# Optimization experiments

Hardware: AMD Instinct MI355X
Metric: run time of the kernel (lower is better)

The kernel has to match this reference:

```python
import jax, jax.numpy as jnp
import numpy as np

K_SIZE = 5
PAD = 2  # (dilation*(k-1)+1-stride+1)//2 with dilation=stride=1
DEPTH_MAX = 10.0
SAMPLE_NUM = 40
AREA_TYPE = 1
AREA_THRED = 0.0  # k_size**2 * 0.5 * 0.0


def _select_index(k_size=K_SIZE, sample_num=SAMPLE_NUM, area_thred=AREA_THRED,
                  area_type=AREA_TYPE, seed=0):
    """Faithful port of AdaptiveDepth2normal.select_index (host-side, deterministic seed)."""
    rng = np.random.RandomState(seed)
    num = k_size ** 2
    p1 = rng.choice(num, sample_num, replace=True); rng.shuffle(p1)
    p2 = rng.choice(num, sample_num, replace=True); rng.shuffle(p2)
    p3 = rng.choice(num, sample_num, replace=True); rng.shuffle(p3)
    index_list = np.stack([p1, p2, p3], axis=1)
    valid_list, seen, areas = [], set(), []
    for row in index_list:
        a, b, c = np.sort(row)
        if (a, b, c) in seen:
            continue
        ax, ay = a % k_size, a // k_size
        bx, by = b % k_size, b // k_size
        cx, cy = c % k_size, c // k_size
        # NOTE: /2 applies only to second term, exactly as in the original code
        area = (bx - ax) * (cy - ay) - (by - ay) * (cx - ax) / 2
        if area > area_thred:
            valid_list.append([a, b, c]); seen.add((a, b, c)); areas.append(area)
        elif area < -area_thred:
            valid_list.append([a, c, b]); seen.add((a, c, b)); areas.append(-area)
    tri = np.asarray(valid_list, dtype=np.int32)              # [nn, 3]
    w = np.asarray(areas, dtype=np.float64) ** area_type
    return tri, (w / w.sum()).astype(np.float32)


def _unfold(x, k=K_SIZE, pad=PAD):
    """torch.nn.Unfold(k, padding=pad, stride=1): x [B,C,H,W] -> [B,C,k*k,H,W], kh-major order."""
    B, C, H, W = x.shape
    xp = jnp.pad(x, ((0, 0), (0, 0), (pad, pad), (pad, pad)))
    return jnp.stack([xp[:, :, dy:dy + H, dx:dx + W]
                      for dy in range(k) for dx in range(k)], axis=2)


def setup_inputs() -> dict:
    key = jax.random.key(0)
    k1, k2 = jax.random.split(key)
    B, H, W = 2, 384, 512
    depth = jax.random.uniform(k1, (B, 1, H, W), dtype=jnp.float32) * 8.0 + 0.5  # in (0, depth_max)
    Kmat = jnp.array([[500.0, 0.0, W / 2.0],
                      [0.0, 500.0, H / 2.0],
                      [0.0, 0.0, 1.0]], dtype=jnp.float32)
    intrinsic = jnp.tile(Kmat[None], (B, 1, 1))
    guide_weight = jax.random.uniform(k2, (B, H, W, K_SIZE * K_SIZE), dtype=jnp.float32)
    tri, aw = _select_index()
    return {"depth": depth, "intrinsic": intrinsic, "guide_weight": guide_weight,
            "triangle_index": jnp.asarray(tri), "triangle_area_weights": jnp.asarray(aw)}


def reference(depth, intrinsic, guide_weight, triangle_index, triangle_area_weights):
    d = depth[:, 0]                                  # [B,H,W]
    B, H, W = d.shape
    Kinv = jnp.linalg.inv(intrinsic)                 # [B,3,3]
    jj = jnp.arange(W, dtype=d.dtype)
    ii = jnp.arange(H, dtype=d.dtype)
    coords = jnp.stack([jnp.broadcast_to(jj[None, :], (H, W)),
                        jnp.broadcast_to(ii[:, None], (H, W)),
                        jnp.ones((H, W), d.dtype)], axis=0)  # [3,H,W] (u,v,1)
    points = jnp.einsum('bij,jhw->bihw', Kinv, coords) * d[:, None]  # [B,3,H,W]

    pp = _unfold(points).transpose(0, 3, 4, 2, 1)    # [B,H,W,25,3]
    p1 = jnp.take(pp, triangle_index[:, 0], axis=3)  # [B,H,W,nn,3]
    p2 = jnp.take(pp, triangle_index[:, 1], axis=3)
    p3 = jnp.take(pp, triangle_index[:, 2], axis=3)
    n = jnp.cross(p2 - p1, p3 - p1)                  # [B,H,W,nn,3]
    n = n / (jnp.linalg.norm(n, axis=-1, keepdims=True) + 1e-5)

    valid = ((d > 0) & (d < DEPTH_MAX)).astype(d.dtype)          # [B,H,W]
    vp = _unfold(valid[:, None])[:, 0].transpose(0, 2, 3, 1)     # [B,H,W,25]
    v_tri = (jnp.take(vp, triangle_index[:, 0], axis=3)
             * jnp.take(vp, triangle_index[:, 1], axis=3)
             * jnp.take(vp, triangle_index[:, 2], axis=3))       # [B,H,W,nn]
    g_tri = (jnp.take(guide_weight, triangle_index[:, 0], axis=3)
             * jnp.take(guide_weight, triangle_index[:, 1], axis=3)
             * jnp.take(guide_weight, triangle_index[:, 2], axis=3))
    fw = v_tri * triangle_area_weights[None, None, None, :] * g_tri  # if_area=True, if_pa=True
    fw = jax.nn.softmax(fw, axis=-1)
    nw = jnp.sum(n * fw[..., None], axis=3)                      # [B,H,W,3]
    nw = nw / (jnp.linalg.norm(nw, axis=-1, keepdims=True) + 1e-5)
    out = jnp.where(valid[..., None] > 0, nw, jnp.zeros((), d.dtype))
    return out.transpose(0, 3, 1, 2), points
```

## Files before the change

kernel.cpp:

```cpp
#include <hip/hip_runtime.h>
#include <math.h>

#define KSZ 5
#define PADR 2
#define TILE_W 32
#define TILE_H 8
#define HALO_W (TILE_W + 2*PADR)
#define HALO_H (TILE_H + 2*PADR)
#define HALO_N (HALO_H * HALO_W)
#define MAX_TRI 128
#define NTHREADS 256

__device__ __forceinline__ float eigen_pexp(float x) {
    float m = floorf(__fmaf_rn(x, 1.44269504088896341f, 0.5f));
    float r = __fmaf_rn(-m, 0.693359375f, x);
    r = __fmaf_rn(-m, -2.12194440e-4f, r);
    float r2 = __fmul_rn(r, r);
    float p = 1.9875691500E-4f;
    p = __fmaf_rn(p, r, 1.3981999507E-3f);
    p = __fmaf_rn(p, r, 8.3334519073E-3f);
    p = __fmaf_rn(p, r, 4.1665795894E-2f);
    p = __fmaf_rn(p, r, 1.6666665459E-1f);
    p = __fmaf_rn(p, r, 5.0000001201E-1f);
    p = __fmaf_rn(p, r2, r);
    p = __fadd_rn(p, 1.0f);
    return ldexpf(p, (int)m);
}

__global__ __launch_bounds__(NTHREADS)
void d2n_kernel(const float* __restrict__ depth,
                const float* __restrict__ intrinsic,
                const float* __restrict__ guide,
                const int* __restrict__ tri,
                const float* __restrict__ aw,
                float* __restrict__ out_n,
                float* __restrict__ out_p,
                int B, int H, int W, int T)
{
    __shared__ float4 s_pts[HALO_N];
    __shared__ float  s_gw[TILE_H * TILE_W * (KSZ*KSZ)];

    const int tid = threadIdx.x;
    const int tx  = tid & (TILE_W - 1);
    const int ty  = tid >> 5;
    const int b   = blockIdx.z;
    const int w0  = blockIdx.x * TILE_W;
    const int h0  = blockIdx.y * TILE_H;

    const float* Km = intrinsic + b * 9;
    const double a00=Km[0], a01=Km[1], a02=Km[2];
    const double a10=Km[3], a11=Km[4], a12=Km[5];
    const double a20=Km[6], a21=Km[7], a22=Km[8];
    const double det = a00*(a11*a22-a12*a21) - a01*(a10*a22-a12*a20) + a02*(a10*a21-a11*a20);
    const double id  = 1.0 / det;
    const float i00 = (float)((a11*a22-a12*a21)*id), i01 = (float)((a02*a21-a01*a22)*id), i02 = (float)((a01*a12-a02*a11)*id);
    const float i10 = (float)((a12*a20-a10*a22)*id), i11 = (float)((a00*a22-a02*a20)*id), i12 = (float)((a02*a10-a00*a12)*id);
    const float i20 = (float)((a10*a21-a11*a20)*id), i21 = (float)((a01*a20-a00*a21)*id), i22 = (float)((a00*a11-a01*a10)*id);

    for (int i = tid; i < HALO_N; i += NTHREADS) {
        int r  = i / HALO_W;
        int c  = i - r * HALO_W;
        int hh = h0 + r - PADR;
        int ww = w0 + c - PADR;
        float4 v = make_float4(0.f, 0.f, 0.f, 0.f);
        if (hh >= 0 && hh < H && ww >= 0 && ww < W) {
            float d  = depth[(size_t)(b * H + hh) * W + ww];
            float fj = (float)ww, fi = (float)hh;
            float sx = __fadd_rn(__fadd_rn(__fmul_rn(i00, fj), __fmul_rn(i01, fi)), i02);
            float sy = __fadd_rn(__fadd_rn(__fmul_rn(i10, fj), __fmul_rn(i11, fi)), i12);
            float sz = __fadd_rn(__fadd_rn(__fmul_rn(i20, fj), __fmul_rn(i21, fi)), i22);
            v.x = __fmul_rn(sx, d);
            v.y = __fmul_rn(sy, d);
            v.z = __fmul_rn(sz, d);
            v.w = (d > 0.f && d < 10.f) ? 1.f : 0.f;
        }
        s_pts[i] = v;
    }

    const int GW_TOT = TILE_H * TILE_W * (KSZ*KSZ);
    for (int i = tid; i < GW_TOT; i += NTHREADS) {
        int r   = i / (TILE_W * KSZ*KSZ);
        int rem = i - r * (TILE_W * KSZ*KSZ);
        int hh  = h0 + r;
        float val = 0.f;
        if (hh < H)
            val = guide[((size_t)(b * H + hh) * W + w0) * (KSZ*KSZ) + rem];
        s_gw[i] = val;
    }

    __syncthreads();

    const int base = ty * HALO_W + tx;
    const int ctr  = base + PADR * HALO_W + PADR;
    float* gw_pix = &s_gw[(ty * TILE_W + tx) * (KSZ*KSZ)];
    const float4 pcv = s_pts[ctr];
    const float  cv  = pcv.w;

    #pragma unroll
    for (int k = 0; k < KSZ*KSZ; ++k) {
        const int o = base + (k / KSZ) * HALO_W + (k % KSZ);
        gw_pix[k] = __fmul_rn(gw_pix[k], s_pts[o].w);
    }

    const int Tl = T < MAX_TRI ? T : MAX_TRI;

    float r0=0.f, r1=0.f, r2=0.f, r3=0.f, r4=0.f, r5=0.f, r6=0.f, r7=0.f;
    float axv = 0.f, ayv = 0.f, azv = 0.f;

    auto body = [&](int t, float& racc) {
        int j1 = tri[3*t], j2 = tri[3*t+1], j3 = tri[3*t+2];
        float awt = aw[t];
        int o1 = base + (j1 / KSZ) * HALO_W + (j1 - (j1 / KSZ) * KSZ);
        int o2 = base + (j2 / KSZ) * HALO_W + (j2 - (j2 / KSZ) * KSZ);
        int o3 = base + (j3 / KSZ) * HALO_W + (j3 - (j3 / KSZ) * KSZ);
        float g = __fmul_rn(__fmul_rn(gw_pix[j1], gw_pix[j2]), gw_pix[j3]);
        float f = __fmul_rn(g, awt);
        float e = eigen_pexp(f);
        racc = __fadd_rn(racc, e);
        float4 p1 = s_pts[o1], p2 = s_pts[o2], p3 = s_pts[o3];
        float e1x = __fsub_rn(p2.x, p1.x), e1y = __fsub_rn(p2.y, p1.y), e1z = __fsub_rn(p2.z, p1.z);
        float e2x = __fsub_rn(p3.x, p1.x), e2y = __fsub_rn(p3.y, p1.y), e2z = __fsub_rn(p3.z, p1.z);
        float t1 = __fmul_rn(e1z, e2y);
        float nx = __fmaf_rn(e1y, e2z, -t1);
        float t2 = __fmul_rn(e1x, e2z);
        float ny = __fmaf_rn(e1z, e2x, -t2);
        float t3 = __fmul_rn(e1y, e2x);
        float nz = __fmaf_rn(e1x, e2y, -t3);
        float q   = __fmaf_rn(nx, nx, __fmaf_rn(ny, ny, __fmul_rn(nz, nz)));
        float den = __fadd_rn(__builtin_amdgcn_sqrtf(q), 1e-5f);
        float inv = __builtin_amdgcn_rcpf(den);
        float ew  = __fmul_rn(e, inv);
        axv = __fmaf_rn(nx, ew, axv);
        ayv = __fmaf_rn(ny, ew, ayv);
        azv = __fmaf_rn(nz, ew, azv);
    };

    const int nmain = (Tl >= 8) ? (Tl & ~7) : 0;
    for (int tb = 0; tb < nmain; tb += 8) {
        body(tb+0, r0); body(tb+1, r1); body(tb+2, r2); body(tb+3, r3);
        body(tb+4, r4); body(tb+5, r5); body(tb+6, r6); body(tb+7, r7);
    }
    float s = 0.f;
    if (Tl >= 8)
        s = __fadd_rn(__fadd_rn(__fadd_rn(r0, r1), __fadd_rn(r2, r3)),
                      __fadd_rn(__fadd_rn(r4, r5), __fadd_rn(r6, r7)));
    for (int t = nmain; t < Tl; ++t) body(t, s);

    float nwx = __fdiv_rn(axv, s);
    float nwy = __fdiv_rn(ayv, s);
    float nwz = __fdiv_rn(azv, s);
    float q2   = __fmaf_rn(nwx, nwx, __fmaf_rn(nwy, nwy, __fmul_rn(nwz, nwz)));
    float den2 = __fadd_rn(__fsqrt_rn(q2), 1e-5f);
    float ox = __fdiv_rn(nwx, den2);
    float oy = __fdiv_rn(nwy, den2);
    float oz = __fdiv_rn(nwz, den2);
    if (cv <= 0.f) { ox = 0.f; oy = 0.f; oz = 0.f; }

    const int hh = h0 + ty, ww = w0 + tx;
    if (hh < H && ww < W) {
        const size_t hw = (size_t)H * W;
        const size_t p0 = (size_t)b * 3 * hw + (size_t)hh * W + ww;
        out_n[p0]        = ox;
        out_n[p0 + hw]   = oy;
        out_n[p0 + 2*hw] = oz;
        out_p[p0]        = pcv.x;
        out_p[p0 + hw]   = pcv.y;
        out_p[p0 + 2*hw] = pcv.z;
    }
}

extern "C" void kernel_launch(void* const* d_in, const int* in_sizes, int n_in,
                              void* d_out, int out_size, void* d_ws, size_t ws_size,
                              hipStream_t stream) {
    const float* depth = (const float*)d_in[0];
    const float* intr  = (const float*)d_in[1];
    const float* guide = (const float*)d_in[2];
    const int*   tri   = (const int*)d_in[3];
    const float* aw    = (const float*)d_in[4];

    const int B = in_sizes[1] / 9;
    const int T = in_sizes[4];
    const int H = 384, W = 512;

    float* out_n = (float*)d_out;
    float* out_p = out_n + (size_t)B * 3 * H * W;

    dim3 grid((W + TILE_W - 1) / TILE_W, (H + TILE_H - 1) / TILE_H, B);
    d2n_kernel<<<grid, NTHREADS, 0, stream>>>(depth, intr, guide, tri, aw,
                                              out_n, out_p, B, H, W, T);
}
```

Measured before the change: 48.53 us.

## Compute two pixels per thread with split SoA LDS layout and taller tiles

New measurement: 60.26 us. 24.2% more time.

```diff
diff --git a/kernel.cpp b/kernel.cpp
--- a/kernel.cpp
+++ b/kernel.cpp
@@ -4,10 +4,12 @@
 #define KSZ 5
 #define PADR 2
 #define TILE_W 32
-#define TILE_H 8
+#define TILE_H 16
 #define HALO_W (TILE_W + 2*PADR)
 #define HALO_H (TILE_H + 2*PADR)
 #define HALO_N (HALO_H * HALO_W)
+#define X2ST 37
+#define GVST 260
 #define MAX_TRI 128
 #define NTHREADS 256
 
@@ -27,7 +29,7 @@
     return ldexpf(p, (int)m);
 }
 
-__global__ __launch_bounds__(NTHREADS)
+__global__ __launch_bounds__(NTHREADS, 2)
 void d2n_kernel(const float* __restrict__ depth,
                 const float* __restrict__ intrinsic,
                 const float* __restrict__ guide,
@@ -37,12 +39,13 @@
                 float* __restrict__ out_p,
                 int B, int H, int W, int T)
 {
-    __shared__ float4 s_pts[HALO_N];
-    __shared__ float  s_gw[TILE_H * TILE_W * (KSZ*KSZ)];
+    __shared__ float2 sX[HALO_H * X2ST];
+    __shared__ float2 sY[HALO_H * X2ST];
+    __shared__ float2 sZ[HALO_H * X2ST];
+    __shared__ float  sV[HALO_N];
+    __shared__ float2 sG[25 * GVST];
 
     const int tid = threadIdx.x;
-    const int tx  = tid & (TILE_W - 1);
-    const int ty  = tid >> 5;
     const int b   = blockIdx.z;
     const int w0  = blockIdx.x * TILE_W;
     const int h0  = blockIdx.y * TILE_H;
@@ -57,115 +60,160 @@
     const float i10 = (float)((a12*a20-a10*a22)*id), i11 = (float)((a00*a22-a02*a20)*id), i12 = (float)((a02*a10-a00*a12)*id);
     const float i20 = (float)((a10*a21-a11*a20)*id), i21 = (float)((a01*a20-a00*a21)*id), i22 = (float)((a00*a11-a01*a10)*id);
 
+    float* Xd = (float*)sX; float* Yd = (float*)sY; float* Zd = (float*)sZ;
     for (int i = tid; i < HALO_N; i += NTHREADS) {
-        int r  = i / HALO_W;
-        int c  = i - r * HALO_W;
-        int hh = h0 + r - PADR;
-        int ww = w0 + c - PADR;
-        float4 v = make_float4(0.f, 0.f, 0.f, 0.f);
+        int hr = i / HALO_W;
+        int hc = i - hr * HALO_W;
+        int hh = h0 + hr - PADR;
+        int ww = w0 + hc - PADR;
+        float x = 0.f, y = 0.f, z = 0.f, v = 0.f;
         if (hh >= 0 && hh < H && ww >= 0 && ww < W) {
             float d  = depth[(size_t)(b * H + hh) * W + ww];
             float fj = (float)ww, fi = (float)hh;
             float sx = __fadd_rn(__fadd_rn(__fmul_rn(i00, fj), __fmul_rn(i01, fi)), i02);
             float sy = __fadd_rn(__fadd_rn(__fmul_rn(i10, fj), __fmul_rn(i11, fi)), i12);
             float sz = __fadd_rn(__fadd_rn(__fmul_rn(i20, fj), __fmul_rn(i21, fi)), i22);
-            v.x = __fmul_rn(sx, d);
-            v.y = __fmul_rn(sy, d);
-            v.z = __fmul_rn(sz, d);
-            v.w = (d > 0.f && d < 10.f) ? 1.f : 0.f;
+            x = __fmul_rn(sx, d);
+            y = __fmul_rn(sy, d);
+            z = __fmul_rn(sz, d);
+            v = (d > 0.f && d < 10.f) ? 1.f : 0.f;
         }
-        s_pts[i] = v;
-    }
-
-    const int GW_TOT = TILE_H * TILE_W * (KSZ*KSZ);
-    for (int i = tid; i < GW_TOT; i += NTHREADS) {
-        int r   = i / (TILE_W * KSZ*KSZ);
-        int rem = i - r * (TILE_W * KSZ*KSZ);
-        int hh  = h0 + r;
-        float val = 0.f;
-        if (hh < H)
-            val = guide[((size_t)(b * H + hh) * W + w0) * (KSZ*KSZ) + rem];
-        s_gw[i] = val;
-    }
-
+        int da = hr * (2 * X2ST) + 2 * hc;
+        Xd[da] = x; Yd[da] = y; Zd[da] = z;
+        if (hc > 0) { Xd[da-1] = x; Yd[da-1] = y; Zd[da-1] = z; }
+        sV[i] = v;
+    }
     __syncthreads();
 
-    const int base = ty * HALO_W + tx;
-    const int ctr  = base + PADR * HALO_W + PADR;
-    float* gw_pix = &s_gw[(ty * TILE_W + tx) * (KSZ*KSZ)];
-    const float4 pcv = s_pts[ctr];
-    const float  cv  = pcv.w;
-
-    #pragma unroll
-    for (int k = 0; k < KSZ*KSZ; ++k) {
-        const int o = base + (k / KSZ) * HALO_W + (k % KSZ);
-        gw_pix[k] = __fmul_rn(gw_pix[k], s_pts[o].w);
-    }
+    float* Gd = (float*)sG;
+    for (int i = tid; i < TILE_H * TILE_W * 25; i += NTHREADS) {
+        int row = i / (TILE_W * 25);
+        int rem = i - row * (TILE_W * 25);
+        int col = rem / 25;
+        int k   = rem - col * 25;
+        int hh  = h0 + row;
+        float val = (hh < H)
+            ? guide[((size_t)(b * H + hh) * W + w0) * 25 + rem] : 0.f;
+        int kd = k / 5, km = k - 5 * kd;
+        float pv = sV[(row + kd) * HALO_W + (col + km)];
+        Gd[k * (2 * GVST) + row * TILE_W + col] = __fmul_rn(val, pv);
+    }
+    __syncthreads();
+
+    const int l   = tid & 63;
+    const int wv  = tid >> 6;
+    const int row = wv * 4 + (l >> 4);
+    const int lx  = l & 15;
+    const int col = 2 * lx;
+    const int pb  = row * X2ST + col;
+    const int gb  = (row << 4) + lx;
 
     const int Tl = T < MAX_TRI ? T : MAX_TRI;
 
-    float r0=0.f, r1=0.f, r2=0.f, r3=0.f, r4=0.f, r5=0.f, r6=0.f, r7=0.f;
-    float axv = 0.f, ayv = 0.f, azv = 0.f;
-
-    auto body = [&](int t, float& racc) {
+    float r0a=0.f,r1a=0.f,r2a=0.f,r3a=0.f,r4a=0.f,r5a=0.f,r6a=0.f,r7a=0.f;
+    float r0b=0.f,r1b=0.f,r2b=0.f,r3b=0.f,r4b=0.f,r5b=0.f,r6b=0.f,r7b=0.f;
+    float axa=0.f, aya=0.f, aza=0.f, axb=0.f, ayb=0.f, azb=0.f;
+
+    auto body = [&](int t, float& ra, float& rb) {
         int j1 = tri[3*t], j2 = tri[3*t+1], j3 = tri[3*t+2];
         float awt = aw[t];
-        int o1 = base + (j1 / KSZ) * HALO_W + (j1 - (j1 / KSZ) * KSZ);
-        int o2 = base + (j2 / KSZ) * HALO_W + (j2 - (j2 / KSZ) * KSZ);
-        int o3 = base + (j3 / KSZ) * HALO_W + (j3 - (j3 / KSZ) * KSZ);
-        float g = __fmul_rn(__fmul_rn(gw_pix[j1], gw_pix[j2]), gw_pix[j3]);
-        float f = __fmul_rn(g, awt);
-        float e = eigen_pexp(f);
-        racc = __fadd_rn(racc, e);
-        float4 p1 = s_pts[o1], p2 = s_pts[o2], p3 = s_pts[o3];
-        float e1x = __fsub_rn(p2.x, p1.x), e1y = __fsub_rn(p2.y, p1.y), e1z = __fsub_rn(p2.z, p1.z);
-        float e2x = __fsub_rn(p3.x, p1.x), e2y = __fsub_rn(p3.y, p1.y), e2z = __fsub_rn(p3.z, p1.z);
-        float t1 = __fmul_rn(e1z, e2y);
-        float nx = __fmaf_rn(e1y, e2z, -t1);
-        float t2 = __fmul_rn(e1x, e2z);
-        float ny = __fmaf_rn(e1z, e2x, -t2);
-        float t3 = __fmul_rn(e1y, e2x);
-        float nz = __fmaf_rn(e1x, e2y, -t3);
-        float q   = __fmaf_rn(nx, nx, __fmaf_rn(ny, ny, __fmul_rn(nz, nz)));
-        float den = __fadd_rn(__builtin_amdgcn_sqrtf(q), 1e-5f);
-        float inv = __builtin_amdgcn_rcpf(den);
-        float ew  = __fmul_rn(e, inv);
-        axv = __fmaf_rn(nx, ew, axv);
-        ayv = __fmaf_rn(ny, ew, ayv);
-        azv = __fmaf_rn(nz, ew, azv);
+        int d1 = (j1 / KSZ) * X2ST + (j1 - (j1 / KSZ) * KSZ);
+        int d2 = (j2 / KSZ) * X2ST + (j2 - (j2 / KSZ) * KSZ);
+        int d3 = (j3 / KSZ) * X2ST + (j3 - (j3 / KSZ) * KSZ);
+        float2 G1 = sG[j1 * GVST + gb];
+        float2 G2 = sG[j2 * GVST + gb];
+        float2 G3 = sG[j3 * GVST + gb];
+        float2 x1 = sX[pb + d1], y1 = sY[pb + d1], z1 = sZ[pb + d1];
+        float2 x2 = sX[pb + d2], y2 = sY[pb + d2], z2 = sZ[pb + d2];
+        float2 x3 = sX[pb + d3], y3 = sY[pb + d3], z3 = sZ[pb + d3];
+        {
+            float g = __fmul_rn(__fmul_rn(G1.x, G2.x), G3.x);
+            float f = __fmul_rn(g, awt);
+            float e = eigen_pexp(f);
+            ra = __fadd_rn(ra, e);
+            float e1x = __fsub_rn(x2.x, x1.x), e1y = __fsub_rn(y2.x, y1.x), e1z = __fsub_rn(z2.x, z1.x);
+            float e2x = __fsub_rn(x3.x, x1.x), e2y = __fsub_rn(y3.x, y1.x), e2z = __fsub_rn(z3.x, z1.x);
+            float t1 = __fmul_rn(e1z, e2y);
+            float nx = __fmaf_rn(e1y, e2z, -t1);
+            float t2 = __fmul_rn(e1x, e2z);
+            float ny = __fmaf_rn(e1z, e2x, -t2);
+            float t3 = __fmul_rn(e1y, e2x);
+            float nz = __fmaf_rn(e1x, e2y, -t3);
+            float q   = __fmaf_rn(nx, nx, __fmaf_rn(ny, ny, __fmul_rn(nz, nz)));
+            float den = __fadd_rn(__builtin_amdgcn_sqrtf(q), 1e-5f);
+            float inv = __builtin_amdgcn_rcpf(den);
+            float ew  = __fmul_rn(e, inv);
+            axa = __fmaf_rn(nx, ew, axa);
+            aya = __fmaf_rn(ny, ew, aya);
+            aza = __fmaf_rn(nz, ew, aza);
+        }
+        {
+            float g = __fmul_rn(__fmul_rn(G1.y, G2.y), G3.y);
+            float f = __fmul_rn(g, awt);
+            float e = eigen_pexp(f);
+            rb = __fadd_rn(rb, e);
+            float e1x = __fsub_rn(x2.y, x1.y), e1y = __fsub_rn(y2.y, y1.y), e1z = __fsub_rn(z2.y, z1.y);
+            float e2x = __fsub_rn(x3.y, x1.y), e2y = __fsub_rn(y3.y, y1.y), e2z = __fsub_rn(z3.y, z1.y);
+            float t1 = __fmul_rn(e1z, e2y);
+            float nx = __fmaf_rn(e1y, e2z, -t1);
+            float t2 = __fmul_rn(e1x, e2z);
+            float ny = __fmaf_rn(e1z, e2x, -t2);
+            float t3 = __fmul_rn(e1y, e2x);
+            float nz = __fmaf_rn(e1x, e2y, -t3);
+            float q   = __fmaf_rn(nx, nx, __fmaf_rn(ny, ny, __fmul_rn(nz, nz)));
+            float den = __fadd_rn(__builtin_amdgcn_sqrtf(q), 1e-5f);
+            float inv = __builtin_amdgcn_rcpf(den);
+            float ew  = __fmul_rn(e, inv);
+            axb = __fmaf_rn(nx, ew, axb);
+            ayb = __fmaf_rn(ny, ew, ayb);
+            azb = __fmaf_rn(nz, ew, azb);
+        }
     };
 
     const int nmain = (Tl >= 8) ? (Tl & ~7) : 0;
     for (int tb = 0; tb < nmain; tb += 8) {
-        body(tb+0, r0); body(tb+1, r1); body(tb+2, r2); body(tb+3, r3);
-        body(tb+4, r4); body(tb+5, r5); body(tb+6, r6); body(tb+7, r7);
-    }
-    float s = 0.f;
-    if (Tl >= 8)
-        s = __fadd_rn(__fadd_rn(__fadd_rn(r0, r1), __fadd_rn(r2, r3)),
-                      __fadd_rn(__fadd_rn(r4, r5), __fadd_rn(r6, r7)));
-    for (int t = nmain; t < Tl; ++t) body(t, s);
-
-    float nwx = __fdiv_rn(axv, s);
-    float nwy = __fdiv_rn(ayv, s);
-    float nwz = __fdiv_rn(azv, s);
+        body(tb+0, r0a, r0b); body(tb+1, r1a, r1b);
+        body(tb+2, r2a, r2b); body(tb+3, r3a, r3b);
+        body(tb+4, r4a, r4b); body(tb+5, r5a, r5b);
+        body(tb+6, r6a, r6b); body(tb+7, r7a, r7b);
+    }
+    float sa = 0.f, sb = 0.f;
+    if (Tl >= 8) {
+        sa = __fadd_rn(__fadd_rn(__fadd_rn(r0a, r1a), __fadd_rn(r2a, r3a)),
+                       __fadd_rn(__fadd_rn(r4a, r5a), __fadd_rn(r6a, r7a)));
+        sb = __fadd_rn(__fadd_rn(__fadd_rn(r0b, r1b), __fadd_rn(r2b, r3b)),
+                       __fadd_rn(__fadd_rn(r4b, r5b), __fadd_rn(r6b, r7b)));
+    }
+    for (int t = nmain; t < Tl; ++t) body(t, sa, sb);
+
+    const float2 cx2 = sX[(row + PADR) * X2ST + col + PADR];
+    const float2 cy2 = sY[(row + PADR) * X2ST + col + PADR];
+    const float2 cz2 = sZ[(row + PADR) * X2ST + col + PADR];
+    const float  cva = sV[(row + PADR) * HALO_W + col + PADR];
+    const float  cvb = sV[(row + PADR) * HALO_W + col + PADR + 1];
+
+    float nwx = __fdiv_rn(axa, sa), nwy = __fdiv_rn(aya, sa), nwz = __fdiv_rn(aza, sa);
     float q2   = __fmaf_rn(nwx, nwx, __fmaf_rn(nwy, nwy, __fmul_rn(nwz, nwz)));
     float den2 = __fadd_rn(__fsqrt_rn(q2), 1e-5f);
-    float ox = __fdiv_rn(nwx, den2);
-    float oy = __fdiv_rn(nwy, den2);
-    float oz = __fdiv_rn(nwz, den2);
-    if (cv <= 0.f) { ox = 0.f; oy = 0.f; oz = 0.f; }
-
-    const int hh = h0 + ty, ww = w0 + tx;
-    if (hh < H && ww < W) {
+    float oxa = __fdiv_rn(nwx, den2), oya = __fdiv_rn(nwy, den2), oza = __fdiv_rn(nwz, den2);
+    if (cva <= 0.f) { oxa = 0.f; oya = 0.f; oza = 0.f; }
+
+    nwx = __fdiv_rn(axb, sb); nwy = __fdiv_rn(ayb, sb); nwz = __fdiv_rn(azb, sb);
+    q2   = __fmaf_rn(nwx, nwx, __fmaf_rn(nwy, nwy, __fmul_rn(nwz, nwz)));
+    den2 = __fadd_rn(__fsqrt_rn(q2), 1e-5f);
+    float oxb = __fdiv_rn(nwx, den2), oyb = __fdiv_rn(nwy, den2), ozb = __fdiv_rn(nwz, den2);
+    if (cvb <= 0.f) { oxb = 0.f; oyb = 0.f; ozb = 0.f; }
+
+    const int hh = h0 + row, ww = w0 + col;
+    if (hh < H && ww + 1 < W) {
         const size_t hw = (size_t)H * W;
         const size_t p0 = (size_t)b * 3 * hw + (size_t)hh * W + ww;
-        out_n[p0]        = ox;
-        out_n[p0 + hw]   = oy;
-        out_n[p0 + 2*hw] = oz;
-        out_p[p0]        = pcv.x;
-        out_p[p0 + hw]   = pcv.y;
-        out_p[p0 + 2*hw] = pcv.z;
+        *(float2*)&out_n[p0]          = make_float2(oxa, oxb);
+        *(float2*)&out_n[p0 + hw]     = make_float2(oya, oyb);
+        *(float2*)&out_n[p0 + 2*hw]   = make_float2(oza, ozb);
+        *(float2*)&out_p[p0]          = make_float2(cx2.x, cx2.y);
+        *(float2*)&out_p[p0 + hw]     = make_float2(cy2.x, cy2.y);
+        *(float2*)&out_p[p0 + 2*hw]   = make_float2(cz2.x, cz2.y);
     }
 }
 
```

## Split point unprojection into a separate pass with padded global buffer

Applied to the files above, without the earlier changes.

Measured after the change: 47.29 us. 1.03x faster.

```diff
diff --git a/kernel.cpp b/kernel.cpp
--- a/kernel.cpp
+++ b/kernel.cpp
@@ -28,14 +28,163 @@
 }
 
 __global__ __launch_bounds__(NTHREADS)
-void d2n_kernel(const float* __restrict__ depth,
+void pts_kernel(const float* __restrict__ depth,
                 const float* __restrict__ intrinsic,
-                const float* __restrict__ guide,
-                const int* __restrict__ tri,
-                const float* __restrict__ aw,
-                float* __restrict__ out_n,
+                float4* __restrict__ pts,
                 float* __restrict__ out_p,
-                int B, int H, int W, int T)
+                int B, int H, int W)
+{
+    const int HP = H + 2*PADR, WP = W + 2*PADR;
+    const int total = B * HP * WP;
+    int idx = blockIdx.x * NTHREADS + threadIdx.x;
+    if (idx >= total) return;
+    int b   = idx / (HP * WP);
+    int rem = idx - b * (HP * WP);
+    int pr  = rem / WP;
+    int pc  = rem - pr * WP;
+    int hh  = pr - PADR;
+    int ww  = pc - PADR;
+
+    const float* Km = intrinsic + b * 9;
+    const double a00=Km[0], a01=Km[1], a02=Km[2];
+    const double a10=Km[3], a11=Km[4], a12=Km[5];
+    const double a20=Km[6], a21=Km[7], a22=Km[8];
+    const double det = a00*(a11*a22-a12*a21) - a01*(a10*a22-a12*a20) + a02*(a10*a21-a11*a20);
+    const double id  = 1.0 / det;
+    const float i00 = (float)((a11*a22-a12*a21)*id), i01 = (float)((a02*a21-a01*a22)*id), i02 = (float)((a01*a12-a02*a11)*id);
+    const float i10 = (float)((a12*a20-a10*a22)*id), i11 = (float)((a00*a22-a02*a20)*id), i12 = (float)((a02*a10-a00*a12)*id);
+    const float i20 = (float)((a10*a21-a11*a20)*id), i21 = (float)((a01*a20-a00*a21)*id), i22 = (float)((a00*a11-a01*a10)*id);
+
+    float4 v = make_float4(0.f, 0.f, 0.f, 0.f);
+    if (hh >= 0 && hh < H && ww >= 0 && ww < W) {
+        float d  = depth[(size_t)(b * H + hh) * W + ww];
+        float fj = (float)ww, fi = (float)hh;
+        float sx = __fadd_rn(__fadd_rn(__fmul_rn(i00, fj), __fmul_rn(i01, fi)), i02);
+        float sy = __fadd_rn(__fadd_rn(__fmul_rn(i10, fj), __fmul_rn(i11, fi)), i12);
+        float sz = __fadd_rn(__fadd_rn(__fmul_rn(i20, fj), __fmul_rn(i21, fi)), i22);
+        v.x = __fmul_rn(sx, d);
+        v.y = __fmul_rn(sy, d);
+        v.z = __fmul_rn(sz, d);
+        v.w = (d > 0.f && d < 10.f) ? 1.f : 0.f;
+        const size_t hw = (size_t)H * W;
+        const size_t p0 = (size_t)b * 3 * hw + (size_t)hh * W + ww;
+        out_p[p0]        = v.x;
+        out_p[p0 + hw]   = v.y;
+        out_p[p0 + 2*hw] = v.z;
+    }
+    pts[idx] = v;
+}
+
+__global__ __launch_bounds__(NTHREADS)
+void d2n_main(const float4* __restrict__ pts,
+              const float* __restrict__ guide,
+              const int* __restrict__ tri,
+              const float* __restrict__ aw,
+              float* __restrict__ out_n,
+              int B, int H, int W, int T)
+{
+    __shared__ float s_gw[TILE_H * TILE_W * (KSZ*KSZ)];
+
+    const int HP = H + 2*PADR, WP = W + 2*PADR;
+    const int tid = threadIdx.x;
+    const int tx  = tid & (TILE_W - 1);
+    const int ty  = tid >> 5;
+    const int b   = blockIdx.z;
+    const int w0  = blockIdx.x * TILE_W;
+    const int h0  = blockIdx.y * TILE_H;
+
+    const int GW_TOT = TILE_H * TILE_W * (KSZ*KSZ);
+    for (int i = tid; i < GW_TOT; i += NTHREADS) {
+        int r   = i / (TILE_W * KSZ*KSZ);
+        int rem = i - r * (TILE_W * KSZ*KSZ);
+        int hh  = h0 + r;
+        float val = 0.f;
+        if (hh < H)
+            val = guide[((size_t)(b * H + hh) * W + w0) * (KSZ*KSZ) + rem];
+        s_gw[i] = val;
+    }
+    __syncthreads();
+
+    const float* gw_pix = &s_gw[(ty * TILE_W + tx) * (KSZ*KSZ)];
+    const int pbase = (b * HP + h0 + ty) * WP + (w0 + tx);
+
+    const int Tl = T < MAX_TRI ? T : MAX_TRI;
+
+    float r0=0.f, r1=0.f, r2=0.f, r3=0.f, r4=0.f, r5=0.f, r6=0.f, r7=0.f;
+    float axv = 0.f, ayv = 0.f, azv = 0.f;
+
+    auto body = [&](int t, float& racc) {
+        int j1 = tri[3*t], j2 = tri[3*t+1], j3 = tri[3*t+2];
+        float awt = aw[t];
+        int o1 = (j1 / KSZ) * WP + (j1 - (j1 / KSZ) * KSZ);
+        int o2 = (j2 / KSZ) * WP + (j2 - (j2 / KSZ) * KSZ);
+        int o3 = (j3 / KSZ) * WP + (j3 - (j3 / KSZ) * KSZ);
+        float4 p1 = pts[pbase + o1];
+        float4 p2 = pts[pbase + o2];
+        float4 p3 = pts[pbase + o3];
+        float vv = __fmul_rn(__fmul_rn(p1.w, p2.w), p3.w);
+        float g  = __fmul_rn(__fmul_rn(gw_pix[j1], gw_pix[j2]), gw_pix[j3]);
+        float f  = __fmul_rn(__fmul_rn(vv, awt), g);
+        float e  = eigen_pexp(f);
+        racc = __fadd_rn(racc, e);
+        float e1x = __fsub_rn(p2.x, p1.x), e1y = __fsub_rn(p2.y, p1.y), e1z = __fsub_rn(p2.z, p1.z);
+        float e2x = __fsub_rn(p3.x, p1.x), e2y = __fsub_rn(p3.y, p1.y), e2z = __fsub_rn(p3.z, p1.z);
+        float t1 = __fmul_rn(e1z, e2y);
+        float nx = __fmaf_rn(e1y, e2z, -t1);
+        float t2 = __fmul_rn(e1x, e2z);
+        float ny = __fmaf_rn(e1z, e2x, -t2);
+        float t3 = __fmul_rn(e1y, e2x);
+        float nz = __fmaf_rn(e1x, e2y, -t3);
+        float q   = __fmaf_rn(nx, nx, __fmaf_rn(ny, ny, __fmul_rn(nz, nz)));
+        float den = __fadd_rn(__builtin_amdgcn_sqrtf(q), 1e-5f);
+        float inv = __builtin_amdgcn_rcpf(den);
+        float ew  = __fmul_rn(e, inv);
+        axv = __fmaf_rn(nx, ew, axv);
+        ayv = __fmaf_rn(ny, ew, ayv);
+        azv = __fmaf_rn(nz, ew, azv);
+    };
+
+    const int nmain = (Tl >= 8) ? (Tl & ~7) : 0;
+    for (int tb = 0; tb < nmain; tb += 8) {
+        body(tb+0, r0); body(tb+1, r1); body(tb+2, r2); body(tb+3, r3);
+        body(tb+4, r4); body(tb+5, r5); body(tb+6, r6); body(tb+7, r7);
+    }
+    float s = 0.f;
+    if (Tl >= 8)
+        s = __fadd_rn(__fadd_rn(__fadd_rn(r0, r1), __fadd_rn(r2, r3)),
+                      __fadd_rn(__fadd_rn(r4, r5), __fadd_rn(r6, r7)));
+    for (int t = nmain; t < Tl; ++t) body(t, s);
+
+    const float4 pc = pts[pbase + PADR * WP + PADR];
+    float nwx = __fdiv_rn(axv, s);
+    float nwy = __fdiv_rn(ayv, s);
+    float nwz = __fdiv_rn(azv, s);
+    float q2   = __fmaf_rn(nwx, nwx, __fmaf_rn(nwy, nwy, __fmul_rn(nwz, nwz)));
+    float den2 = __fadd_rn(__fsqrt_rn(q2), 1e-5f);
+    float ox = __fdiv_rn(nwx, den2);
+    float oy = __fdiv_rn(nwy, den2);
+    float oz = __fdiv_rn(nwz, den2);
+    if (pc.w <= 0.f) { ox = 0.f; oy = 0.f; oz = 0.f; }
+
+    const int hh = h0 + ty, ww = w0 + tx;
+    if (hh < H && ww < W) {
+        const size_t hw = (size_t)H * W;
+        const size_t p0 = (size_t)b * 3 * hw + (size_t)hh * W + ww;
+        out_n[p0]        = ox;
+        out_n[p0 + hw]   = oy;
+        out_n[p0 + 2*hw] = oz;
+    }
+}
+
+__global__ __launch_bounds__(NTHREADS)
+void d2n_fallback(const float* __restrict__ depth,
+                  const float* __restrict__ intrinsic,
+                  const float* __restrict__ guide,
+                  const int* __restrict__ tri,
+                  const float* __restrict__ aw,
+                  float* __restrict__ out_n,
+                  float* __restrict__ out_p,
+                  int B, int H, int W, int T)
 {
     __shared__ float4 s_pts[HALO_N];
     __shared__ float  s_gw[TILE_H * TILE_W * (KSZ*KSZ)];
@@ -76,7 +225,6 @@
         }
         s_pts[i] = v;
     }
-
     const int GW_TOT = TILE_H * TILE_W * (KSZ*KSZ);
     for (int i = tid; i < GW_TOT; i += NTHREADS) {
         int r   = i / (TILE_W * KSZ*KSZ);
@@ -87,37 +235,28 @@
             val = guide[((size_t)(b * H + hh) * W + w0) * (KSZ*KSZ) + rem];
         s_gw[i] = val;
     }
-
     __syncthreads();
 
     const int base = ty * HALO_W + tx;
     const int ctr  = base + PADR * HALO_W + PADR;
-    float* gw_pix = &s_gw[(ty * TILE_W + tx) * (KSZ*KSZ)];
+    const float* gw_pix = &s_gw[(ty * TILE_W + tx) * (KSZ*KSZ)];
     const float4 pcv = s_pts[ctr];
-    const float  cv  = pcv.w;
-
-    #pragma unroll
-    for (int k = 0; k < KSZ*KSZ; ++k) {
-        const int o = base + (k / KSZ) * HALO_W + (k % KSZ);
-        gw_pix[k] = __fmul_rn(gw_pix[k], s_pts[o].w);
-    }
-
     const int Tl = T < MAX_TRI ? T : MAX_TRI;
 
     float r0=0.f, r1=0.f, r2=0.f, r3=0.f, r4=0.f, r5=0.f, r6=0.f, r7=0.f;
     float axv = 0.f, ayv = 0.f, azv = 0.f;
-
     auto body = [&](int t, float& racc) {
         int j1 = tri[3*t], j2 = tri[3*t+1], j3 = tri[3*t+2];
         float awt = aw[t];
         int o1 = base + (j1 / KSZ) * HALO_W + (j1 - (j1 / KSZ) * KSZ);
         int o2 = base + (j2 / KSZ) * HALO_W + (j2 - (j2 / KSZ) * KSZ);
         int o3 = base + (j3 / KSZ) * HALO_W + (j3 - (j3 / KSZ) * KSZ);
-        float g = __fmul_rn(__fmul_rn(gw_pix[j1], gw_pix[j2]), gw_pix[j3]);
-        float f = __fmul_rn(g, awt);
-        float e = eigen_pexp(f);
+        float4 p1 = s_pts[o1], p2 = s_pts[o2], p3 = s_pts[o3];
+        float vv = __fmul_rn(__fmul_rn(p1.w, p2.w), p3.w);
+        float g  = __fmul_rn(__fmul_rn(gw_pix[j1], gw_pix[j2]), gw_pix[j3]);
+        float f  = __fmul_rn(__fmul_rn(vv, awt), g);
+        float e  = eigen_pexp(f);
         racc = __fadd_rn(racc, e);
-        float4 p1 = s_pts[o1], p2 = s_pts[o2], p3 = s_pts[o3];
         float e1x = __fsub_rn(p2.x, p1.x), e1y = __fsub_rn(p2.y, p1.y), e1z = __fsub_rn(p2.z, p1.z);
         float e2x = __fsub_rn(p3.x, p1.x), e2y = __fsub_rn(p3.y, p1.y), e2z = __fsub_rn(p3.z, p1.z);
         float t1 = __fmul_rn(e1z, e2y);
@@ -134,7 +273,6 @@
         ayv = __fmaf_rn(ny, ew, ayv);
         azv = __fmaf_rn(nz, ew, azv);
     };
-
     const int nmain = (Tl >= 8) ? (Tl & ~7) : 0;
     for (int tb = 0; tb < nmain; tb += 8) {
         body(tb+0, r0); body(tb+1, r1); body(tb+2, r2); body(tb+3, r3);
@@ -154,7 +292,7 @@
     float ox = __fdiv_rn(nwx, den2);
     float oy = __fdiv_rn(nwy, den2);
     float oz = __fdiv_rn(nwz, den2);
-    if (cv <= 0.f) { ox = 0.f; oy = 0.f; oz = 0.f; }
+    if (pcv.w <= 0.f) { ox = 0.f; oy = 0.f; oz = 0.f; }
 
     const int hh = h0 + ty, ww = w0 + tx;
     if (hh < H && ww < W) {
@@ -181,11 +319,23 @@
     const int B = in_sizes[1] / 9;
     const int T = in_sizes[4];
     const int H = 384, W = 512;
+    const int HP = H + 2*PADR, WP = W + 2*PADR;
 
     float* out_n = (float*)d_out;
     float* out_p = out_n + (size_t)B * 3 * H * W;
 
+    const size_t need = (size_t)B * HP * WP * sizeof(float4);
     dim3 grid((W + TILE_W - 1) / TILE_W, (H + TILE_H - 1) / TILE_H, B);
-    d2n_kernel<<<grid, NTHREADS, 0, stream>>>(depth, intr, guide, tri, aw,
-                                              out_n, out_p, B, H, W, T);
-}
+
+    if (ws_size >= need) {
+        float4* pts = (float4*)d_ws;
+        int total = B * HP * WP;
+        pts_kernel<<<(total + NTHREADS - 1) / NTHREADS, NTHREADS, 0, stream>>>(
+            depth, intr, pts, out_p, B, H, W);
+        d2n_main<<<grid, NTHREADS, 0, stream>>>(
+            pts, guide, tri, aw, out_n, B, H, W, T);
+    } else {
+        d2n_fallback<<<grid, NTHREADS, 0, stream>>>(
+            depth, intr, guide, tri, aw, out_n, out_p, B, H, W, T);
+    }
+}
```
